# Kernel optimization log

Measured on AMD Instinct MI355X. Metric: run time of the kernel, lower is better.

## Reference

```python
import jax, jax.numpy as jnp
import numpy as np

B, M, C, S, SD, K, H = 32, 448, 384, 512, 128, 8, 8
DH = C // H
EPS = 1e-5
NEG_SLOPE = 0.2


def setup_inputs() -> dict:
    key = jax.random.key(0)
    ks = iter(jax.random.split(key, 32))
    nrm = lambda shape, scale=0.05: (jax.random.normal(next(ks), shape, jnp.float32) * scale)
    inp = {
        'q': jax.random.normal(next(ks), (B, M, C), jnp.float32),
        'coarse': jax.random.normal(next(ks), (B, M, 3), jnp.float32),
        'skeleton': jax.random.normal(next(ks), (B, S, 3), jnp.float32),
        # GraphConv 1: 3 -> 64 (root weight, rel/neighbor weight, bias)
        'gc1_wroot': nrm((3, 64), 0.3), 'gc1_wrel': nrm((3, 64), 0.3), 'gc1_b': jnp.zeros((64,), jnp.float32),
        # GraphConv 2: 64 -> SD
        'gc2_wroot': nrm((64, SD), 0.1), 'gc2_wrel': nrm((64, SD), 0.1), 'gc2_b': jnp.zeros((SD,), jnp.float32),
        # skeleton_projection: SD -> C
        'proj_w': nrm((SD, C), 0.08), 'proj_b': jnp.zeros((C,), jnp.float32),
        # MultiheadAttention (torch layout: in_proj (3C, C), out_proj (C, C))
        'attn_in_w': nrm((3 * C, C), 0.05), 'attn_in_b': jnp.zeros((3 * C,), jnp.float32),
        'attn_out_w': nrm((C, C), 0.05), 'attn_out_b': jnp.zeros((C,), jnp.float32),
        # increase_dim: Conv1d(C,1024,1) + BN(1024) + LeakyReLU + Conv1d(1024,1024,1)
        'inc1_w': nrm((1024, C), 0.05), 'inc1_b': jnp.zeros((1024,), jnp.float32),
        'bn_g': jnp.ones((1024,), jnp.float32), 'bn_b': jnp.zeros((1024,), jnp.float32),
        'bn_m': jnp.zeros((1024,), jnp.float32), 'bn_v': jnp.ones((1024,), jnp.float32),
        'inc2_w': nrm((1024, 1024), 0.03), 'inc2_b': jnp.zeros((1024,), jnp.float32),
        # reduce_map: Linear(C + 1024 + 3, C)
        'red_w': nrm((1024 + C + 3, C), 0.03), 'red_b': jnp.zeros((C,), jnp.float32),
    }
    return inp


def _knn_idx(pts):
    # pts: [B,S,3]; per-batch kNN (self excluded), matching knn_graph(k=K, batch=...)
    d2 = jnp.sum((pts[:, :, None, :] - pts[:, None, :, :]) ** 2, axis=-1)  # [B,S,S]
    d2 = d2 + jnp.eye(S, dtype=pts.dtype)[None] * 1e10                       # mask self
    _, idx = jax.lax.top_k(-d2, K)                                           # [B,S,K]
    return idx


def _graph_conv(x, idx, wroot, wrel, b):
    # GraphConv (PyG, aggr='add'): out_i = x_i Wroot + (sum_{j in N(i)} x_j) Wrel + b
    nb = jax.vmap(lambda f, i: f[i])(x, idx)   # [B,S,K,F]
    agg = nb.sum(axis=2)                       # [B,S,F]
    return x @ wroot + agg @ wrel + b


def reference(q, coarse, skeleton, gc1_wroot, gc1_wrel, gc1_b, gc2_wroot, gc2_wrel, gc2_b,
              proj_w, proj_b, attn_in_w, attn_in_b, attn_out_w, attn_out_b,
              inc1_w, inc1_b, bn_g, bn_b, bn_m, bn_v, inc2_w, inc2_b, red_w, red_b):
    # --- skeleton branch: knn graph + 2-layer GraphConv + max-pool + projection ---
    idx = _knn_idx(skeleton)
    h = _graph_conv(skeleton, idx, gc1_wroot, gc1_wrel, gc1_b)
    h = jax.nn.relu(h)
    h = _graph_conv(h, idx, gc2_wroot, gc2_wrel, gc2_b)        # [B,S,SD]
    proxy = jnp.max(h, axis=1)                                  # [B,SD]
    proxy = proxy @ proj_w + proj_b                             # [B,C]
    kv = jnp.broadcast_to(proxy[:, None, :], (B, M, C))         # expanded proxies

    # --- cross attention (torch nn.MultiheadAttention math) ---
    wq, wk, wv = attn_in_w[:C], attn_in_w[C:2 * C], attn_in_w[2 * C:]
    bq, bk, bv = attn_in_b[:C], attn_in_b[C:2 * C], attn_in_b[2 * C:]
    qh = (q @ wq.T + bq).reshape(B, M, H, DH)
    kh = (kv @ wk.T + bk).reshape(B, M, H, DH)
    vh = (kv @ wv.T + bv).reshape(B, M, H, DH)
    scores = jnp.einsum('bmhd,bnhd->bhmn', qh, kh) / jnp.sqrt(jnp.float32(DH))
    attn = jax.nn.softmax(scores, axis=-1)
    ctx = jnp.einsum('bhmn,bnhd->bmhd', attn, vh).reshape(B, M, C)
    q = ctx @ attn_out_w.T + attn_out_b                         # fused features [B,M,C]

    # --- increase_dim (1x1 conv == matmul) + BN(eval) + LeakyReLU + 1x1 conv ---
    g = jnp.einsum('bmc,oc->bmo', q, inc1_w) + inc1_b           # [B,M,1024]
    g = bn_g * (g - bn_m) * jax.lax.rsqrt(bn_v + EPS) + bn_b
    g = jnp.where(g >= 0, g, NEG_SLOPE * g)
    g = jnp.einsum('bmc,oc->bmo', g, inc2_w) + inc2_b
    global_feature = jnp.max(g, axis=1)                         # [B,1024]

    # --- concat + reduce_map ---
    rebuild = jnp.concatenate([jnp.broadcast_to(global_feature[:, None, :], (B, M, 1024)), q, coarse], axis=-1)
    out = rebuild @ red_w + red_b                               # [B,M,C]
    return out
```

## Files before the change

kernel.cpp:

```cpp
#include <hip/hip_runtime.h>

#define NB 32
#define MM 448
#define CC 384
#define SS 512
#define KNN 8

#define WS_IDX   0u
#define WS_H1    524288u
#define WS_PMAX  (WS_H1 + 4194304u)
#define WS_Q     (WS_PMAX + 262144u)
#define WS_Y     (WS_Q + 49152u)
#define WS_G2    (WS_Y + 131072u)
#define WS_BASEP (WS_G2 + 131072u)
#define WS_PP    WS_H1
#define WS_KV    WS_IDX
#define WS_VV    (WS_IDX + 49152u)

__device__ __forceinline__ float wave_sum(float v) {
#pragma unroll
  for (int m = 1; m < 64; m <<= 1) v += __shfl_xor(v, m, 64);
  return v;
}

__global__ __launch_bounds__(256) void k_knn_gc1(
    const float* __restrict__ skel,
    const float* __restrict__ w1root, const float* __restrict__ w1rel,
    const float* __restrict__ b1,
    int* __restrict__ idx_ws, float* __restrict__ h1_ws)
{
  int b   = blockIdx.x >> 7;
  int grp = blockIdx.x & 127;
  __shared__ __align__(16) float4 sk[SS];
  const float* sb = skel + b * SS * 3;
  for (int t = threadIdx.x; t < SS; t += 256)
    sk[t] = make_float4(sb[t*3+0], sb[t*3+1], sb[t*3+2], 0.f);
  __syncthreads();

  int wave = threadIdx.x >> 6, lane = threadIdx.x & 63;
  int i = grp * 4 + wave;
  float4 pi = sk[i];

  float bd[KNN];
#pragma unroll
  for (int t = 0; t < KNN; t++) {
    int j = lane + (t << 6);
    float4 p = sk[j];
    float d2;
    {
#pragma clang fp contract(off)
      float dx = pi.x - p.x, dy = pi.y - p.y, dz = pi.z - p.z;
      d2 = (dx*dx + dy*dy) + dz*dz;
    }
    bd[t] = (j == i) ? 3e38f : d2;
  }

  int win[KNN];
  int* idx_base = idx_ws + (size_t)(b*SS + i) * KNN;
#pragma unroll
  for (int t = 0; t < KNN; t++) {
    float bestd = bd[0]; int bests = 0;
#pragma unroll
    for (int s = 1; s < KNN; s++)
      if (bd[s] < bestd) { bestd = bd[s]; bests = s; }
    int bestj = lane + (bests << 6);
#pragma unroll
    for (int m = 1; m < 64; m <<= 1) {
      float od = __shfl_xor(bestd, m, 64);
      int   oj = __shfl_xor(bestj, m, 64);
      if (od < bestd || (od == bestd && oj < bestj)) { bestd = od; bestj = oj; }
    }
    win[t] = bestj;
    if (lane == t) idx_base[t] = bestj;
    if ((bestj & 63) == lane) {
      int sl = bestj >> 6;
#pragma unroll
      for (int s = 0; s < KNN; s++) if (s == sl) bd[s] = 3e38f;
    }
  }

  float a0 = 0.f, a1 = 0.f, a2 = 0.f;
#pragma unroll
  for (int t = 0; t < KNN; t++) {
    float4 n = sk[win[t]];
    a0 += n.x; a1 += n.y; a2 += n.z;
  }

  int c = lane;
  float h = b1[c] + pi.x*w1root[c] + pi.y*w1root[64+c] + pi.z*w1root[128+c]
                  + a0*w1rel[c]   + a1*w1rel[64+c]   + a2*w1rel[128+c];
  h = fmaxf(h, 0.f);
  h1_ws[(size_t)(b*SS + i) * 64 + lane] = h;
}

__global__ __launch_bounds__(256) void k_gc2_max(
    const float* __restrict__ h1_ws, const int* __restrict__ idx_ws,
    const float* __restrict__ w2root, const float* __restrict__ w2rel,
    const float* __restrict__ b2, float* __restrict__ pmax)
{
  int b = blockIdx.x >> 4, chunk = blockIdx.x & 15;
  int r0 = chunk * 32;
  __shared__ __align__(16) float X[32*129];
  __shared__ __align__(16) float Wt[32*128];
  __shared__ float mred[8*128];
  __shared__ int nbs[32*KNN];

  const float* h1b = h1_ws + (size_t)b * SS * 64;
  nbs[threadIdx.x] = idx_ws[(b*SS + r0)*KNN + threadIdx.x];
#pragma unroll
  for (int p = 0; p < 8; p++) {
    int idx = threadIdx.x + 256*p;
    int r = idx >> 6, k = idx & 63;
    X[r*129 + k] = h1b[(r0 + r)*64 + k];
  }
  __syncthreads();
#pragma unroll
  for (int p = 0; p < 8; p++) {
    int idx = threadIdx.x + 256*p;
    int r = idx >> 6, k = idx & 63;
    const int* nb = nbs + r*KNN;
    float s = 0.f;
#pragma unroll
    for (int j = 0; j < KNN; j++) s += h1b[nb[j]*64 + k];
    X[r*129 + 64 + k] = s;
  }

  int rg = threadIdx.x >> 5, cg = threadIdx.x & 31;
  float acc[4][4];
#pragma unroll
  for (int r = 0; r < 4; r++)
#pragma unroll
    for (int u = 0; u < 4; u++) acc[r][u] = 0.f;

  const float* wsrc[4] = { w2root, w2root + 32*128, w2rel, w2rel + 32*128 };
#pragma unroll 1
  for (int ch = 0; ch < 4; ch++) {
    __syncthreads();
    const float* ws = wsrc[ch];
#pragma unroll
    for (int p = 0; p < 16; p++) {
      int idx = threadIdx.x + 256*p;
      Wt[idx] = ws[idx];
    }
    __syncthreads();
    int kb = ch * 32;
    const float* xr0 = X + (rg*4+0)*129 + kb;
    const float* xr1 = X + (rg*4+1)*129 + kb;
    const float* xr2 = X + (rg*4+2)*129 + kb;
    const float* xr3 = X + (rg*4+3)*129 + kb;
#pragma unroll 4
    for (int k = 0; k < 32; k++) {
      float4 w4 = *(const float4*)(Wt + k*128 + cg*4);
      float x0 = xr0[k], x1 = xr1[k], x2 = xr2[k], x3 = xr3[k];
      acc[0][0] += x0*w4.x; acc[0][1] += x0*w4.y; acc[0][2] += x0*w4.z; acc[0][3] += x0*w4.w;
      acc[1][0] += x1*w4.x; acc[1][1] += x1*w4.y; acc[1][2] += x1*w4.z; acc[1][3] += x1*w4.w;
      acc[2][0] += x2*w4.x; acc[2][1] += x2*w4.y; acc[2][2] += x2*w4.z; acc[2][3] += x2*w4.w;
      acc[3][0] += x3*w4.x; acc[3][1] += x3*w4.y; acc[3][2] += x3*w4.z; acc[3][3] += x3*w4.w;
    }
  }
#pragma unroll
  for (int u = 0; u < 4; u++)
    mred[rg*128 + cg*4 + u] =
      fmaxf(fmaxf(acc[0][u], acc[1][u]), fmaxf(acc[2][u], acc[3][u]));
  __syncthreads();
  if (threadIdx.x < 128) {
    int col = threadIdx.x;
    float mx = mred[col];
#pragma unroll
    for (int g = 1; g < 8; g++) mx = fmaxf(mx, mred[g*128 + col]);
    pmax[(size_t)(b*16 + chunk)*128 + col] = mx + b2[col];
  }
}

__global__ __launch_bounds__(384) void k_proxy_kv(
    const float* __restrict__ pmax,
    const float* __restrict__ proj_w, const float* __restrict__ proj_b,
    float* __restrict__ kv_ws)
{
  int b = blockIdx.x, t = threadIdx.x;
  __shared__ float proxy[128];
  if (t < 128) {
    float m = -3e38f;
    for (int ch = 0; ch < 16; ch++) m = fmaxf(m, pmax[(size_t)(b*16 + ch)*128 + t]);
    proxy[t] = m;
  }
  __syncthreads();
  float acc = proj_b[t];
  for (int s = 0; s < 128; s++) acc += proxy[s] * proj_w[s*CC + t];
  kv_ws[b*CC + t] = acc;
}

__global__ __launch_bounds__(256) void k_mv384(
    const float* __restrict__ xin, const float* __restrict__ w, int row0,
    const float* __restrict__ bias, int bias0, float* __restrict__ out)
{
  int b = blockIdx.x, og = blockIdx.y;
  int wv = threadIdx.x >> 6, lane = threadIdx.x & 63;
  __shared__ float xs[CC];
  for (int t = threadIdx.x; t < CC; t += 256) xs[t] = xin[b*CC + t];
  __syncthreads();
  float x0 = xs[lane*6+0], x1 = xs[lane*6+1], x2 = xs[lane*6+2];
  float x3 = xs[lane*6+3], x4 = xs[lane*6+4], x5 = xs[lane*6+5];
#pragma unroll
  for (int u = 0; u < 8; u++) {
    int o = og*32 + wv*8 + u;
    const float* wr = w + (size_t)(row0 + o) * CC + lane*6;
    float2 wa = *(const float2*)wr;
    float2 wb = *(const float2*)(wr + 2);
    float2 wc = *(const float2*)(wr + 4);
    float p = wa.x*x0 + wa.y*x1 + wb.x*x2 + wb.y*x3 + wc.x*x4 + wc.y*x5;
    p = wave_sum(p);
    if (lane == 0) out[b*CC + o] = bias[bias0 + o] + p;
  }
}

__global__ __launch_bounds__(256) void k_inc1_bn(
    const float* __restrict__ q_ws, const float* __restrict__ inc1_w,
    const float* __restrict__ inc1_b,
    const float* __restrict__ bng, const float* __restrict__ bnb,
    const float* __restrict__ bnm, const float* __restrict__ bnv,
    float* __restrict__ y_ws)
{
  int b = blockIdx.x >> 4, og = blockIdx.x & 15;
  int t = threadIdx.x;
  int o = og*64 + (t >> 2), qq = t & 3;
  __shared__ __align__(16) float xs[CC];
  for (int i = t; i < CC; i += 256) xs[i] = q_ws[b*CC + i];
  __syncthreads();
  const float* wr = inc1_w + (size_t)o * CC + qq*96;
  const float* xr = xs + qq*96;
  float acc = 0.f;
#pragma unroll
  for (int kk = 0; kk < 96; kk += 4) {
    float4 w4 = *(const float4*)(wr + kk);
    float4 x4 = *(const float4*)(xr + kk);
    acc += w4.x*x4.x + w4.y*x4.y + w4.z*x4.z + w4.w*x4.w;
  }
  acc += __shfl_xor(acc, 1, 64);
  acc += __shfl_xor(acc, 2, 64);
  if (qq == 0) {
    float a = acc + inc1_b[o];
    float z = bng[o] * (a - bnm[o]) * rsqrtf(bnv[o] + 1e-5f) + bnb[o];
    y_ws[b*1024 + o] = (z >= 0.f) ? z : 0.2f * z;
  }
}

__global__ __launch_bounds__(256) void k_inc2(
    const float* __restrict__ y_ws, const float* __restrict__ inc2_w,
    const float* __restrict__ inc2_b, float* __restrict__ g2_ws)
{
  int b = blockIdx.x >> 4, og = blockIdx.x & 15;
  int t = threadIdx.x;
  int o = og*64 + (t >> 2), qq = t & 3;
  __shared__ __align__(16) float xs[1024];
  for (int i = t; i < 1024; i += 256) xs[i] = y_ws[b*1024 + i];
  __syncthreads();
  const float* wr = inc2_w + (size_t)o * 1024 + qq*256;
  const float* xr = xs + qq*256;
  float acc = 0.f;
#pragma unroll 8
  for (int kk = 0; kk < 256; kk += 4) {
    float4 w4 = *(const float4*)(wr + kk);
    float4 x4 = *(const float4*)(xr + kk);
    acc += w4.x*x4.x + w4.y*x4.y + w4.z*x4.z + w4.w*x4.w;
  }
  acc += __shfl_xor(acc, 1, 64);
  acc += __shfl_xor(acc, 2, 64);
  if (qq == 0) g2_ws[b*1024 + o] = acc + inc2_b[o];
}

__global__ __launch_bounds__(256) void k_basep(
    const float* __restrict__ g2_ws, const float* __restrict__ q_ws,
    const float* __restrict__ red_w, float* __restrict__ pp)
{
  int cg = blockIdx.x;
  int o0 = blockIdx.y * 64;
  int c0 = cg * 32;
  __shared__ __align__(16) float xs[32*33];
  __shared__ __align__(16) float wt[32*64];
#pragma unroll
  for (int p = 0; p < 8; p++) {
    int idx = threadIdx.x + 256*p;
    int c = idx >> 6, o = idx & 63;
    wt[idx] = red_w[(size_t)(c0 + c)*CC + o0 + o];
  }
  {
    int b = threadIdx.x >> 3, cp = threadIdx.x & 7;
    const float* src = (cg < 32) ? (g2_ws + b*1024 + c0)
                                 : (q_ws  + b*CC   + (c0 - 1024));
    float4 v = *(const float4*)(src + cp*4);
    xs[(cp*4+0)*33 + b] = v.x;
    xs[(cp*4+1)*33 + b] = v.y;
    xs[(cp*4+2)*33 + b] = v.z;
    xs[(cp*4+3)*33 + b] = v.w;
  }
  __syncthreads();
  int b = threadIdx.x >> 3, og = threadIdx.x & 7;
  float acc[8];
#pragma unroll
  for (int u = 0; u < 8; u++) acc[u] = 0.f;
#pragma unroll 8
  for (int c = 0; c < 32; c++) {
    float xv = xs[c*33 + b];
    float4 w0 = *(const float4*)(wt + c*64 + og*8);
    float4 w1 = *(const float4*)(wt + c*64 + og*8 + 4);
    acc[0] += xv*w0.x; acc[1] += xv*w0.y; acc[2] += xv*w0.z; acc[3] += xv*w0.w;
    acc[4] += xv*w1.x; acc[5] += xv*w1.y; acc[6] += xv*w1.z; acc[7] += xv*w1.w;
  }
  float* dst = pp + (size_t)(cg*32 + b)*CC + o0 + og*8;
  *(float4*)dst       = make_float4(acc[0], acc[1], acc[2], acc[3]);
  *(float4*)(dst + 4) = make_float4(acc[4], acc[5], acc[6], acc[7]);
}

__global__ __launch_bounds__(256) void k_base_red(
    const float* __restrict__ pp, float* __restrict__ basep)
{
  int idx = blockIdx.x * 256 + threadIdx.x;
  float s = 0.f;
#pragma unroll 4
  for (int cg = 0; cg < 44; cg++) s += pp[cg*12288 + idx];
  basep[idx] = s;
}

__global__ __launch_bounds__(256) void k_out(
    const float* __restrict__ basep, const float* __restrict__ red_b,
    const float* __restrict__ red_w, const float* __restrict__ coarse,
    float* __restrict__ out)
{
  int gid = blockIdx.x * 256 + threadIdx.x;
  int c4 = gid % 96;
  int row = gid / 96;
  int b = row / 448;
  int c = c4 * 4;
  float4 p0 = *(const float4*)(basep + b*CC + c);
  float4 rb = *(const float4*)(red_b + c);
  const float* cr = coarse + (size_t)row * 3;
  float cx = cr[0], cy = cr[1], cz = cr[2];
  float4 w0 = *(const float4*)(red_w + (size_t)1408*CC + c);
  float4 w1 = *(const float4*)(red_w + (size_t)1409*CC + c);
  float4 w2 = *(const float4*)(red_w + (size_t)1410*CC + c);
  float4 o4;
  o4.x = p0.x + rb.x + cx*w0.x + cy*w1.x + cz*w2.x;
  o4.y = p0.y + rb.y + cx*w0.y + cy*w1.y + cz*w2.y;
  o4.z = p0.z + rb.z + cx*w0.z + cy*w1.z + cz*w2.z;
  o4.w = p0.w + rb.w + cx*w0.w + cy*w1.w + cz*w2.w;
  *(float4*)(out + (size_t)row*CC + c) = o4;
}

extern "C" void kernel_launch(void* const* d_in, const int* in_sizes, int n_in,
                              void* d_out, int out_size, void* d_ws, size_t ws_size,
                              hipStream_t stream)
{
  (void)in_sizes; (void)n_in; (void)out_size; (void)ws_size;
  const float* coarse = (const float*)d_in[1];
  const float* skel   = (const float*)d_in[2];
  const float* g1wr   = (const float*)d_in[3];
  const float* g1wl   = (const float*)d_in[4];
  const float* g1b    = (const float*)d_in[5];
  const float* g2wr   = (const float*)d_in[6];
  const float* g2wl   = (const float*)d_in[7];
  const float* g2b    = (const float*)d_in[8];
  const float* projw  = (const float*)d_in[9];
  const float* projb  = (const float*)d_in[10];
  const float* aiw    = (const float*)d_in[11];
  const float* aib    = (const float*)d_in[12];
  const float* aow    = (const float*)d_in[13];
  const float* aob    = (const float*)d_in[14];
  const float* i1w    = (const float*)d_in[15];
  const float* i1b    = (const float*)d_in[16];
  const float* bng    = (const float*)d_in[17];
  const float* bnb    = (const float*)d_in[18];
  const float* bnm    = (const float*)d_in[19];
  const float* bnv    = (const float*)d_in[20];
  const float* i2w    = (const float*)d_in[21];
  const float* i2b    = (const float*)d_in[22];
  const float* redw   = (const float*)d_in[23];
  const float* redb   = (const float*)d_in[24];
  float* out = (float*)d_out;

  char* ws = (char*)d_ws;
  int*   idx_ws = (int*)(ws + WS_IDX);
  float* h1_ws  = (float*)(ws + WS_H1);
  float* pmax   = (float*)(ws + WS_PMAX);
  float* q_ws   = (float*)(ws + WS_Q);
  float* y_ws   = (float*)(ws + WS_Y);
  float* g2_ws  = (float*)(ws + WS_G2);
  float* basep  = (float*)(ws + WS_BASEP);
  float* pp     = (float*)(ws + WS_PP);
  float* kv_ws  = (float*)(ws + WS_KV);
  float* vv_ws  = (float*)(ws + WS_VV);

  k_knn_gc1<<<4096, 256, 0, stream>>>(skel, g1wr, g1wl, g1b, idx_ws, h1_ws);
  k_gc2_max<<<512, 256, 0, stream>>>(h1_ws, idx_ws, g2wr, g2wl, g2b, pmax);
  k_proxy_kv<<<32, 384, 0, stream>>>(pmax, projw, projb, kv_ws);
  k_mv384<<<dim3(32, 12), 256, 0, stream>>>(kv_ws, aiw, 2*CC, aib, 2*CC, vv_ws);
  k_mv384<<<dim3(32, 12), 256, 0, stream>>>(vv_ws, aow, 0,    aob, 0,    q_ws);
  k_inc1_bn<<<512, 256, 0, stream>>>(q_ws, i1w, i1b, bng, bnb, bnm, bnv, y_ws);
  k_inc2<<<512, 256, 0, stream>>>(y_ws, i2w, i2b, g2_ws);
  k_basep<<<dim3(44, 6), 256, 0, stream>>>(g2_ws, q_ws, redw, pp);
  k_base_red<<<48, 256, 0, stream>>>(pp, basep);
  k_out<<<5376, 256, 0, stream>>>(basep, redb, redw, coarse, out);
}
```

Measured before the change: 236.0 us.

## Fuse post-kNN stages into one persistent kernel with software grid barriers

Nine launches after the kNN/GraphConv1 kernel are merged into one 512-block kernel whose stages are separated by atomic-counter grid barriers. The aim is to remove per-launch overhead and tail gaps between small dependent kernels. The reduce_map partial-sum scheme (44 chunks written out, then a separate reduction) is replaced by 48 blocks that each loop over the full concatenated input, writing the reduction directly. The software barrier assumes all 512 blocks are co-resident, which launch_bounds(256,2) is meant to make likely on this GPU. Barrier spinning and poorly utilised stages (48 active blocks) are the costs taken on.

```diff
diff --git a/kernel.cpp b/kernel.cpp
--- a/kernel.cpp
+++ b/kernel.cpp
@@ -5,30 +5,49 @@
 #define CC 384
 #define SS 512
 #define KNN 8
-
-#define WS_IDX   0u
-#define WS_H1    524288u
-#define WS_PMAX  (WS_H1 + 4194304u)
-#define WS_Q     (WS_PMAX + 262144u)
-#define WS_Y     (WS_Q + 49152u)
-#define WS_G2    (WS_Y + 131072u)
-#define WS_BASEP (WS_G2 + 131072u)
-#define WS_PP    WS_H1
-#define WS_KV    WS_IDX
-#define WS_VV    (WS_IDX + 49152u)
+#define NBLK 512u
+
+#define WS_IDX    0u
+#define WS_H1     524288u
+#define WS_PMAX   4718592u
+#define WS_VV     4980736u
+#define WS_Y      5029888u
+#define WS_XCAT   5160960u
+#define WS_BASEP  5341184u
+#define WS_BAR    5390336u
 
 __device__ __forceinline__ float wave_sum(float v) {
 #pragma unroll
   for (int m = 1; m < 64; m <<= 1) v += __shfl_xor(v, m, 64);
   return v;
+}
+
+__device__ __forceinline__ void gbar(unsigned* c) {
+  __threadfence();
+  __syncthreads();
+  if (threadIdx.x == 0) {
+    __hip_atomic_fetch_add(c, 1u, __ATOMIC_RELEASE, __HIP_MEMORY_SCOPE_AGENT);
+    long spins = 0;
+    unsigned v;
+    do {
+      v = __hip_atomic_load(c, __ATOMIC_ACQUIRE, __HIP_MEMORY_SCOPE_AGENT);
+      if (v >= NBLK) break;
+      __builtin_amdgcn_s_sleep(1);
+    } while (++spins < (1L << 27));
+  }
+  __syncthreads();
+  __threadfence();
 }
 
 __global__ __launch_bounds__(256) void k_knn_gc1(
     const float* __restrict__ skel,
     const float* __restrict__ w1root, const float* __restrict__ w1rel,
     const float* __restrict__ b1,
-    int* __restrict__ idx_ws, float* __restrict__ h1_ws)
+    int* __restrict__ idx_ws, float* __restrict__ h1_ws,
+    unsigned* __restrict__ bar)
 {
+  if (blockIdx.x == 0 && threadIdx.x < 6) bar[threadIdx.x * 16] = 0u;
+
   int b   = blockIdx.x >> 7;
   int grp = blockIdx.x & 127;
   __shared__ __align__(16) float4 sk[SS];
@@ -93,258 +112,264 @@
   h1_ws[(size_t)(b*SS + i) * 64 + lane] = h;
 }
 
-__global__ __launch_bounds__(256) void k_gc2_max(
-    const float* __restrict__ h1_ws, const int* __restrict__ idx_ws,
-    const float* __restrict__ w2root, const float* __restrict__ w2rel,
-    const float* __restrict__ b2, float* __restrict__ pmax)
+struct CoopArgs {
+  const float* h1; const int* idx;
+  const float *g2wr, *g2wl, *g2b;
+  const float *projw, *projb;
+  const float *aiw, *aib, *aow, *aob;
+  const float *i1w, *i1b, *bng, *bnb, *bnm, *bnv;
+  const float *i2w, *i2b;
+  const float *redw, *redb;
+  const float* coarse;
+  float *pmax, *vv, *y, *xcat, *basep, *out;
+  unsigned* bar;
+};
+
+__global__ __launch_bounds__(256, 2) void k_fused(CoopArgs a)
 {
-  int b = blockIdx.x >> 4, chunk = blockIdx.x & 15;
-  int r0 = chunk * 32;
-  __shared__ __align__(16) float X[32*129];
-  __shared__ __align__(16) float Wt[32*128];
-  __shared__ float mred[8*128];
-  __shared__ int nbs[32*KNN];
-
-  const float* h1b = h1_ws + (size_t)b * SS * 64;
-  nbs[threadIdx.x] = idx_ws[(b*SS + r0)*KNN + threadIdx.x];
-#pragma unroll
-  for (int p = 0; p < 8; p++) {
-    int idx = threadIdx.x + 256*p;
-    int r = idx >> 6, k = idx & 63;
-    X[r*129 + k] = h1b[(r0 + r)*64 + k];
-  }
-  __syncthreads();
-#pragma unroll
-  for (int p = 0; p < 8; p++) {
-    int idx = threadIdx.x + 256*p;
-    int r = idx >> 6, k = idx & 63;
-    const int* nb = nbs + r*KNN;
-    float s = 0.f;
-#pragma unroll
-    for (int j = 0; j < KNN; j++) s += h1b[nb[j]*64 + k];
-    X[r*129 + 64 + k] = s;
-  }
-
-  int rg = threadIdx.x >> 5, cg = threadIdx.x & 31;
-  float acc[4][4];
-#pragma unroll
-  for (int r = 0; r < 4; r++)
-#pragma unroll
-    for (int u = 0; u < 4; u++) acc[r][u] = 0.f;
-
-  const float* wsrc[4] = { w2root, w2root + 32*128, w2rel, w2rel + 32*128 };
+  __shared__ __align__(16) float smem[9600];
+  const int t   = threadIdx.x;
+  const int blk = blockIdx.x;
+
+  {
+    int b = blk >> 4, chunk = blk & 15;
+    int r0 = chunk * 32;
+    float* X    = smem;
+    float* Wt   = smem + 4128;
+    float* mred = smem + 8224;
+    int*   nbs  = (int*)(smem + 9248);
+
+    const float* h1b = a.h1 + (size_t)b * SS * 64;
+    nbs[t] = a.idx[(b*SS + r0)*KNN + t];
+#pragma unroll
+    for (int p = 0; p < 8; p++) {
+      int idx = t + 256*p;
+      int r = idx >> 6, k = idx & 63;
+      X[r*129 + k] = h1b[(r0 + r)*64 + k];
+    }
+    __syncthreads();
+#pragma unroll
+    for (int p = 0; p < 8; p++) {
+      int idx = t + 256*p;
+      int r = idx >> 6, k = idx & 63;
+      const int* nb = nbs + r*KNN;
+      float s = 0.f;
+#pragma unroll
+      for (int j = 0; j < KNN; j++) s += h1b[nb[j]*64 + k];
+      X[r*129 + 64 + k] = s;
+    }
+
+    int rg = t >> 5, cgi = t & 31;
+    float acc[4][4];
+#pragma unroll
+    for (int r = 0; r < 4; r++)
+#pragma unroll
+      for (int u = 0; u < 4; u++) acc[r][u] = 0.f;
+
+    const float* wsrc[4] = { a.g2wr, a.g2wr + 32*128, a.g2wl, a.g2wl + 32*128 };
 #pragma unroll 1
-  for (int ch = 0; ch < 4; ch++) {
-    __syncthreads();
-    const float* ws = wsrc[ch];
-#pragma unroll
-    for (int p = 0; p < 16; p++) {
-      int idx = threadIdx.x + 256*p;
-      Wt[idx] = ws[idx];
-    }
-    __syncthreads();
-    int kb = ch * 32;
-    const float* xr0 = X + (rg*4+0)*129 + kb;
-    const float* xr1 = X + (rg*4+1)*129 + kb;
-    const float* xr2 = X + (rg*4+2)*129 + kb;
-    const float* xr3 = X + (rg*4+3)*129 + kb;
+    for (int ch = 0; ch < 4; ch++) {
+      __syncthreads();
+      const float* ws = wsrc[ch];
+#pragma unroll
+      for (int p = 0; p < 16; p++) {
+        int idx = t + 256*p;
+        Wt[idx] = ws[idx];
+      }
+      __syncthreads();
+      int kb = ch * 32;
+      const float* xr0 = X + (rg*4+0)*129 + kb;
+      const float* xr1 = X + (rg*4+1)*129 + kb;
+      const float* xr2 = X + (rg*4+2)*129 + kb;
+      const float* xr3 = X + (rg*4+3)*129 + kb;
 #pragma unroll 4
-    for (int k = 0; k < 32; k++) {
-      float4 w4 = *(const float4*)(Wt + k*128 + cg*4);
-      float x0 = xr0[k], x1 = xr1[k], x2 = xr2[k], x3 = xr3[k];
-      acc[0][0] += x0*w4.x; acc[0][1] += x0*w4.y; acc[0][2] += x0*w4.z; acc[0][3] += x0*w4.w;
-      acc[1][0] += x1*w4.x; acc[1][1] += x1*w4.y; acc[1][2] += x1*w4.z; acc[1][3] += x1*w4.w;
-      acc[2][0] += x2*w4.x; acc[2][1] += x2*w4.y; acc[2][2] += x2*w4.z; acc[2][3] += x2*w4.w;
-      acc[3][0] += x3*w4.x; acc[3][1] += x3*w4.y; acc[3][2] += x3*w4.z; acc[3][3] += x3*w4.w;
-    }
-  }
-#pragma unroll
-  for (int u = 0; u < 4; u++)
-    mred[rg*128 + cg*4 + u] =
-      fmaxf(fmaxf(acc[0][u], acc[1][u]), fmaxf(acc[2][u], acc[3][u]));
-  __syncthreads();
-  if (threadIdx.x < 128) {
-    int col = threadIdx.x;
-    float mx = mred[col];
-#pragma unroll
-    for (int g = 1; g < 8; g++) mx = fmaxf(mx, mred[g*128 + col]);
-    pmax[(size_t)(b*16 + chunk)*128 + col] = mx + b2[col];
-  }
-}
-
-__global__ __launch_bounds__(384) void k_proxy_kv(
-    const float* __restrict__ pmax,
-    const float* __restrict__ proj_w, const float* __restrict__ proj_b,
-    float* __restrict__ kv_ws)
-{
-  int b = blockIdx.x, t = threadIdx.x;
-  __shared__ float proxy[128];
-  if (t < 128) {
-    float m = -3e38f;
-    for (int ch = 0; ch < 16; ch++) m = fmaxf(m, pmax[(size_t)(b*16 + ch)*128 + t]);
-    proxy[t] = m;
-  }
-  __syncthreads();
-  float acc = proj_b[t];
-  for (int s = 0; s < 128; s++) acc += proxy[s] * proj_w[s*CC + t];
-  kv_ws[b*CC + t] = acc;
-}
-
-__global__ __launch_bounds__(256) void k_mv384(
-    const float* __restrict__ xin, const float* __restrict__ w, int row0,
-    const float* __restrict__ bias, int bias0, float* __restrict__ out)
-{
-  int b = blockIdx.x, og = blockIdx.y;
-  int wv = threadIdx.x >> 6, lane = threadIdx.x & 63;
-  __shared__ float xs[CC];
-  for (int t = threadIdx.x; t < CC; t += 256) xs[t] = xin[b*CC + t];
-  __syncthreads();
-  float x0 = xs[lane*6+0], x1 = xs[lane*6+1], x2 = xs[lane*6+2];
-  float x3 = xs[lane*6+3], x4 = xs[lane*6+4], x5 = xs[lane*6+5];
-#pragma unroll
-  for (int u = 0; u < 8; u++) {
-    int o = og*32 + wv*8 + u;
-    const float* wr = w + (size_t)(row0 + o) * CC + lane*6;
-    float2 wa = *(const float2*)wr;
-    float2 wb = *(const float2*)(wr + 2);
-    float2 wc = *(const float2*)(wr + 4);
-    float p = wa.x*x0 + wa.y*x1 + wb.x*x2 + wb.y*x3 + wc.x*x4 + wc.y*x5;
-    p = wave_sum(p);
-    if (lane == 0) out[b*CC + o] = bias[bias0 + o] + p;
-  }
-}
-
-__global__ __launch_bounds__(256) void k_inc1_bn(
-    const float* __restrict__ q_ws, const float* __restrict__ inc1_w,
-    const float* __restrict__ inc1_b,
-    const float* __restrict__ bng, const float* __restrict__ bnb,
-    const float* __restrict__ bnm, const float* __restrict__ bnv,
-    float* __restrict__ y_ws)
-{
-  int b = blockIdx.x >> 4, og = blockIdx.x & 15;
-  int t = threadIdx.x;
-  int o = og*64 + (t >> 2), qq = t & 3;
-  __shared__ __align__(16) float xs[CC];
-  for (int i = t; i < CC; i += 256) xs[i] = q_ws[b*CC + i];
-  __syncthreads();
-  const float* wr = inc1_w + (size_t)o * CC + qq*96;
-  const float* xr = xs + qq*96;
-  float acc = 0.f;
-#pragma unroll
-  for (int kk = 0; kk < 96; kk += 4) {
-    float4 w4 = *(const float4*)(wr + kk);
-    float4 x4 = *(const float4*)(xr + kk);
-    acc += w4.x*x4.x + w4.y*x4.y + w4.z*x4.z + w4.w*x4.w;
-  }
-  acc += __shfl_xor(acc, 1, 64);
-  acc += __shfl_xor(acc, 2, 64);
-  if (qq == 0) {
-    float a = acc + inc1_b[o];
-    float z = bng[o] * (a - bnm[o]) * rsqrtf(bnv[o] + 1e-5f) + bnb[o];
-    y_ws[b*1024 + o] = (z >= 0.f) ? z : 0.2f * z;
-  }
-}
-
-__global__ __launch_bounds__(256) void k_inc2(
-    const float* __restrict__ y_ws, const float* __restrict__ inc2_w,
-    const float* __restrict__ inc2_b, float* __restrict__ g2_ws)
-{
-  int b = blockIdx.x >> 4, og = blockIdx.x & 15;
-  int t = threadIdx.x;
-  int o = og*64 + (t >> 2), qq = t & 3;
-  __shared__ __align__(16) float xs[1024];
-  for (int i = t; i < 1024; i += 256) xs[i] = y_ws[b*1024 + i];
-  __syncthreads();
-  const float* wr = inc2_w + (size_t)o * 1024 + qq*256;
-  const float* xr = xs + qq*256;
-  float acc = 0.f;
+      for (int k = 0; k < 32; k++) {
+        float4 w4 = *(const float4*)(Wt + k*128 + cgi*4);
+        float x0 = xr0[k], x1 = xr1[k], x2 = xr2[k], x3 = xr3[k];
+        acc[0][0] += x0*w4.x; acc[0][1] += x0*w4.y; acc[0][2] += x0*w4.z; acc[0][3] += x0*w4.w;
+        acc[1][0] += x1*w4.x; acc[1][1] += x1*w4.y; acc[1][2] += x1*w4.z; acc[1][3] += x1*w4.w;
+        acc[2][0] += x2*w4.x; acc[2][1] += x2*w4.y; acc[2][2] += x2*w4.z; acc[2][3] += x2*w4.w;
+        acc[3][0] += x3*w4.x; acc[3][1] += x3*w4.y; acc[3][2] += x3*w4.z; acc[3][3] += x3*w4.w;
+      }
+    }
+#pragma unroll
+    for (int u = 0; u < 4; u++)
+      mred[rg*128 + cgi*4 + u] =
+        fmaxf(fmaxf(acc[0][u], acc[1][u]), fmaxf(acc[2][u], acc[3][u]));
+    __syncthreads();
+    if (t < 128) {
+      float mx = mred[t];
+#pragma unroll
+      for (int g = 1; g < 8; g++) mx = fmaxf(mx, mred[g*128 + t]);
+      a.pmax[(size_t)(b*16 + chunk)*128 + t] = mx + a.g2b[t];
+    }
+  }
+  gbar(a.bar + 0*16);
+
+  if (blk < 384) {
+    int b = blk & 31, og = blk >> 5;
+    if (t < 128) {
+      float m = -3e38f;
+      for (int ch = 0; ch < 16; ch++)
+        m = fmaxf(m, a.pmax[(size_t)(b*16 + ch)*128 + t]);
+      smem[t] = m;
+    }
+    __syncthreads();
+    for (int o = t; o < CC; o += 256) {
+      float acc = a.projb[o];
+      for (int s = 0; s < 128; s++) acc += smem[s] * a.projw[s*CC + o];
+      smem[128 + o] = acc;
+    }
+    __syncthreads();
+    const float* xs = smem + 128;
+    int wv = t >> 6, lane = t & 63;
+    float x0 = xs[lane*6+0], x1 = xs[lane*6+1], x2 = xs[lane*6+2];
+    float x3 = xs[lane*6+3], x4 = xs[lane*6+4], x5 = xs[lane*6+5];
+#pragma unroll
+    for (int u = 0; u < 8; u++) {
+      int o = og*32 + wv*8 + u;
+      const float* wr = a.aiw + (size_t)(2*CC + o) * CC + lane*6;
+      float2 wa = *(const float2*)wr;
+      float2 wb = *(const float2*)(wr + 2);
+      float2 wc = *(const float2*)(wr + 4);
+      float p = wa.x*x0 + wa.y*x1 + wb.x*x2 + wb.y*x3 + wc.x*x4 + wc.y*x5;
+      p = wave_sum(p);
+      if (lane == 0) a.vv[b*CC + o] = a.aib[2*CC + o] + p;
+    }
+  }
+  gbar(a.bar + 1*16);
+
+  if (blk < 384) {
+    int b = blk & 31, og = blk >> 5;
+    for (int i = t; i < CC; i += 256) smem[i] = a.vv[b*CC + i];
+    __syncthreads();
+    int wv = t >> 6, lane = t & 63;
+    float x0 = smem[lane*6+0], x1 = smem[lane*6+1], x2 = smem[lane*6+2];
+    float x3 = smem[lane*6+3], x4 = smem[lane*6+4], x5 = smem[lane*6+5];
+#pragma unroll
+    for (int u = 0; u < 8; u++) {
+      int o = og*32 + wv*8 + u;
+      const float* wr = a.aow + (size_t)o * CC + lane*6;
+      float2 wa = *(const float2*)wr;
+      float2 wb = *(const float2*)(wr + 2);
+      float2 wc = *(const float2*)(wr + 4);
+      float p = wa.x*x0 + wa.y*x1 + wb.x*x2 + wb.y*x3 + wc.x*x4 + wc.y*x5;
+      p = wave_sum(p);
+      if (lane == 0) a.xcat[b*1408 + 1024 + o] = a.aob[o] + p;
+    }
+  }
+  gbar(a.bar + 2*16);
+
+  {
+    int b = blk >> 4, og = blk & 15;
+    int o = og*64 + (t >> 2), qq = t & 3;
+    for (int i = t; i < CC; i += 256) smem[i] = a.xcat[b*1408 + 1024 + i];
+    __syncthreads();
+    const float* wr = a.i1w + (size_t)o * CC + qq*96;
+    const float* xr = smem + qq*96;
+    float acc = 0.f;
+#pragma unroll
+    for (int kk = 0; kk < 96; kk += 4) {
+      float4 w4 = *(const float4*)(wr + kk);
+      float4 x4 = *(const float4*)(xr + kk);
+      acc += w4.x*x4.x + w4.y*x4.y + w4.z*x4.z + w4.w*x4.w;
+    }
+    acc += __shfl_xor(acc, 1, 64);
+    acc += __shfl_xor(acc, 2, 64);
+    if (qq == 0) {
+      float v = acc + a.i1b[o];
+      float z = a.bng[o] * (v - a.bnm[o]) * rsqrtf(a.bnv[o] + 1e-5f) + a.bnb[o];
+      a.y[b*1024 + o] = (z >= 0.f) ? z : 0.2f * z;
+    }
+  }
+  gbar(a.bar + 3*16);
+
+  {
+    int b = blk >> 4, og = blk & 15;
+    int o = og*64 + (t >> 2), qq = t & 3;
+    for (int i = t; i < 1024; i += 256) smem[i] = a.y[b*1024 + i];
+    __syncthreads();
+    const float* wr = a.i2w + (size_t)o * 1024 + qq*256;
+    const float* xr = smem + qq*256;
+    float acc = 0.f;
 #pragma unroll 8
-  for (int kk = 0; kk < 256; kk += 4) {
-    float4 w4 = *(const float4*)(wr + kk);
-    float4 x4 = *(const float4*)(xr + kk);
-    acc += w4.x*x4.x + w4.y*x4.y + w4.z*x4.z + w4.w*x4.w;
-  }
-  acc += __shfl_xor(acc, 1, 64);
-  acc += __shfl_xor(acc, 2, 64);
-  if (qq == 0) g2_ws[b*1024 + o] = acc + inc2_b[o];
-}
-
-__global__ __launch_bounds__(256) void k_basep(
-    const float* __restrict__ g2_ws, const float* __restrict__ q_ws,
-    const float* __restrict__ red_w, float* __restrict__ pp)
-{
-  int cg = blockIdx.x;
-  int o0 = blockIdx.y * 64;
-  int c0 = cg * 32;
-  __shared__ __align__(16) float xs[32*33];
-  __shared__ __align__(16) float wt[32*64];
-#pragma unroll
-  for (int p = 0; p < 8; p++) {
-    int idx = threadIdx.x + 256*p;
-    int c = idx >> 6, o = idx & 63;
-    wt[idx] = red_w[(size_t)(c0 + c)*CC + o0 + o];
-  }
+    for (int kk = 0; kk < 256; kk += 4) {
+      float4 w4 = *(const float4*)(wr + kk);
+      float4 x4 = *(const float4*)(xr + kk);
+      acc += w4.x*x4.x + w4.y*x4.y + w4.z*x4.z + w4.w*x4.w;
+    }
+    acc += __shfl_xor(acc, 1, 64);
+    acc += __shfl_xor(acc, 2, 64);
+    if (qq == 0) a.xcat[b*1408 + o] = acc + a.i2b[o];
+  }
+  gbar(a.bar + 4*16);
+
+  if (blk < 48) {
+    int o0 = blk * 8;
+    float* xs = smem;
+    float* wt = smem + 4128;
+    int o4 = t & 1, bb = (t >> 1) & 31, kq = t >> 6;
+    float acc0 = 0.f, acc1 = 0.f, acc2 = 0.f, acc3 = 0.f;
+#pragma unroll 1
+    for (int c0 = 0; c0 < 1408; c0 += 128) {
+      __syncthreads();
+#pragma unroll
+      for (int p = 0; p < 16; p++) {
+        int idx = t + 256*p;
+        xs[(idx >> 7)*129 + (idx & 127)] = a.xcat[(idx >> 7)*1408 + c0 + (idx & 127)];
+      }
+#pragma unroll
+      for (int p = 0; p < 4; p++) {
+        int idx = t + 256*p;
+        wt[idx] = a.redw[(size_t)(c0 + (idx >> 3)) * CC + o0 + (idx & 7)];
+      }
+      __syncthreads();
+      const float* xrow = xs + bb*129 + kq*32;
+      const float* wrow = wt + kq*32*8 + o4*4;
+#pragma unroll 8
+      for (int i = 0; i < 32; i++) {
+        float  x  = xrow[i];
+        float4 w4 = *(const float4*)(wrow + i*8);
+        acc0 += x*w4.x; acc1 += x*w4.y; acc2 += x*w4.z; acc3 += x*w4.w;
+      }
+    }
+    __syncthreads();
+    float* red = smem;
+    red[t*4+0] = acc0; red[t*4+1] = acc1; red[t*4+2] = acc2; red[t*4+3] = acc3;
+    __syncthreads();
+    {
+      int bb2 = t >> 3, oj = t & 7;
+      float s = 0.f;
+#pragma unroll
+      for (int k2 = 0; k2 < 4; k2++)
+        s += red[(k2*64 + bb2*2 + (oj >> 2))*4 + (oj & 3)];
+      a.basep[bb2*CC + o0 + oj] = s;
+    }
+  }
+  gbar(a.bar + 5*16);
+
   {
-    int b = threadIdx.x >> 3, cp = threadIdx.x & 7;
-    const float* src = (cg < 32) ? (g2_ws + b*1024 + c0)
-                                 : (q_ws  + b*CC   + (c0 - 1024));
-    float4 v = *(const float4*)(src + cp*4);
-    xs[(cp*4+0)*33 + b] = v.x;
-    xs[(cp*4+1)*33 + b] = v.y;
-    xs[(cp*4+2)*33 + b] = v.z;
-    xs[(cp*4+3)*33 + b] = v.w;
-  }
-  __syncthreads();
-  int b = threadIdx.x >> 3, og = threadIdx.x & 7;
-  float acc[8];
-#pragma unroll
-  for (int u = 0; u < 8; u++) acc[u] = 0.f;
-#pragma unroll 8
-  for (int c = 0; c < 32; c++) {
-    float xv = xs[c*33 + b];
-    float4 w0 = *(const float4*)(wt + c*64 + og*8);
-    float4 w1 = *(const float4*)(wt + c*64 + og*8 + 4);
-    acc[0] += xv*w0.x; acc[1] += xv*w0.y; acc[2] += xv*w0.z; acc[3] += xv*w0.w;
-    acc[4] += xv*w1.x; acc[5] += xv*w1.y; acc[6] += xv*w1.z; acc[7] += xv*w1.w;
-  }
-  float* dst = pp + (size_t)(cg*32 + b)*CC + o0 + og*8;
-  *(float4*)dst       = make_float4(acc[0], acc[1], acc[2], acc[3]);
-  *(float4*)(dst + 4) = make_float4(acc[4], acc[5], acc[6], acc[7]);
-}
-
-__global__ __launch_bounds__(256) void k_base_red(
-    const float* __restrict__ pp, float* __restrict__ basep)
-{
-  int idx = blockIdx.x * 256 + threadIdx.x;
-  float s = 0.f;
-#pragma unroll 4
-  for (int cg = 0; cg < 44; cg++) s += pp[cg*12288 + idx];
-  basep[idx] = s;
-}
-
-__global__ __launch_bounds__(256) void k_out(
-    const float* __restrict__ basep, const float* __restrict__ red_b,
-    const float* __restrict__ red_w, const float* __restrict__ coarse,
-    float* __restrict__ out)
-{
-  int gid = blockIdx.x * 256 + threadIdx.x;
-  int c4 = gid % 96;
-  int row = gid / 96;
-  int b = row / 448;
-  int c = c4 * 4;
-  float4 p0 = *(const float4*)(basep + b*CC + c);
-  float4 rb = *(const float4*)(red_b + c);
-  const float* cr = coarse + (size_t)row * 3;
-  float cx = cr[0], cy = cr[1], cz = cr[2];
-  float4 w0 = *(const float4*)(red_w + (size_t)1408*CC + c);
-  float4 w1 = *(const float4*)(red_w + (size_t)1409*CC + c);
-  float4 w2 = *(const float4*)(red_w + (size_t)1410*CC + c);
-  float4 o4;
-  o4.x = p0.x + rb.x + cx*w0.x + cy*w1.x + cz*w2.x;
-  o4.y = p0.y + rb.y + cx*w0.y + cy*w1.y + cz*w2.y;
-  o4.z = p0.z + rb.z + cx*w0.z + cy*w1.z + cz*w2.z;
-  o4.w = p0.w + rb.w + cx*w0.w + cy*w1.w + cz*w2.w;
-  *(float4*)(out + (size_t)row*CC + c) = o4;
+    const int total = NB*MM*96;
+    for (int gid = blk*256 + t; gid < total; gid += (int)NBLK*256) {
+      int c4 = gid % 96;
+      int row = gid / 96;
+      int b = row / 448;
+      int c = c4 * 4;
+      float4 p0 = *(const float4*)(a.basep + b*CC + c);
+      float4 rb = *(const float4*)(a.redb + c);
+      const float* cr = a.coarse + (size_t)row * 3;
+      float cx = cr[0], cy = cr[1], cz = cr[2];
+      float4 w0 = *(const float4*)(a.redw + (size_t)1408*CC + c);
+      float4 w1 = *(const float4*)(a.redw + (size_t)1409*CC + c);
+      float4 w2 = *(const float4*)(a.redw + (size_t)1410*CC + c);
+      float4 o4v;
+      o4v.x = p0.x + rb.x + cx*w0.x + cy*w1.x + cz*w2.x;
+      o4v.y = p0.y + rb.y + cx*w0.y + cy*w1.y + cz*w2.y;
+      o4v.z = p0.z + rb.z + cx*w0.z + cy*w1.z + cz*w2.z;
+      o4v.w = p0.w + rb.w + cx*w0.w + cy*w1.w + cz*w2.w;
+      *(float4*)(a.out + (size_t)row*CC + c) = o4v;
+    }
+  }
 }
 
 extern "C" void kernel_launch(void* const* d_in, const int* in_sizes, int n_in,
@@ -357,47 +382,43 @@
   const float* g1wr   = (const float*)d_in[3];
   const float* g1wl   = (const float*)d_in[4];
   const float* g1b    = (const float*)d_in[5];
-  const float* g2wr   = (const float*)d_in[6];
-  const float* g2wl   = (const float*)d_in[7];
-  const float* g2b    = (const float*)d_in[8];
-  const float* projw  = (const float*)d_in[9];
-  const float* projb  = (const float*)d_in[10];
-  const float* aiw    = (const float*)d_in[11];
-  const float* aib    = (const float*)d_in[12];
-  const float* aow    = (const float*)d_in[13];
-  const float* aob    = (const float*)d_in[14];
-  const float* i1w    = (const float*)d_in[15];
-  const float* i1b    = (const float*)d_in[16];
-  const float* bng    = (const float*)d_in[17];
-  const float* bnb    = (const float*)d_in[18];
-  const float* bnm    = (const float*)d_in[19];
-  const float* bnv    = (const float*)d_in[20];
-  const float* i2w    = (const float*)d_in[21];
-  const float* i2b    = (const float*)d_in[22];
-  const float* redw   = (const float*)d_in[23];
-  const float* redb   = (const float*)d_in[24];
-  float* out = (float*)d_out;
 
   char* ws = (char*)d_ws;
-  int*   idx_ws = (int*)(ws + WS_IDX);
-  float* h1_ws  = (float*)(ws + WS_H1);
-  float* pmax   = (float*)(ws + WS_PMAX);
-  float* q_ws   = (float*)(ws + WS_Q);
-  float* y_ws   = (float*)(ws + WS_Y);
-  float* g2_ws  = (float*)(ws + WS_G2);
-  float* basep  = (float*)(ws + WS_BASEP);
-  float* pp     = (float*)(ws + WS_PP);
-  float* kv_ws  = (float*)(ws + WS_KV);
-  float* vv_ws  = (float*)(ws + WS_VV);
-
-  k_knn_gc1<<<4096, 256, 0, stream>>>(skel, g1wr, g1wl, g1b, idx_ws, h1_ws);
-  k_gc2_max<<<512, 256, 0, stream>>>(h1_ws, idx_ws, g2wr, g2wl, g2b, pmax);
-  k_proxy_kv<<<32, 384, 0, stream>>>(pmax, projw, projb, kv_ws);
-  k_mv384<<<dim3(32, 12), 256, 0, stream>>>(kv_ws, aiw, 2*CC, aib, 2*CC, vv_ws);
-  k_mv384<<<dim3(32, 12), 256, 0, stream>>>(vv_ws, aow, 0,    aob, 0,    q_ws);
-  k_inc1_bn<<<512, 256, 0, stream>>>(q_ws, i1w, i1b, bng, bnb, bnm, bnv, y_ws);
-  k_inc2<<<512, 256, 0, stream>>>(y_ws, i2w, i2b, g2_ws);
-  k_basep<<<dim3(44, 6), 256, 0, stream>>>(g2_ws, q_ws, redw, pp);
-  k_base_red<<<48, 256, 0, stream>>>(pp, basep);
-  k_out<<<5376, 256, 0, stream>>>(basep, redb, redw, coarse, out);
+  int*      idx_ws = (int*)(ws + WS_IDX);
+  float*    h1_ws  = (float*)(ws + WS_H1);
+  unsigned* bar    = (unsigned*)(ws + WS_BAR);
+
+  CoopArgs a;
+  a.h1    = h1_ws;
+  a.idx   = idx_ws;
+  a.g2wr  = (const float*)d_in[6];
+  a.g2wl  = (const float*)d_in[7];
+  a.g2b   = (const float*)d_in[8];
+  a.projw = (const float*)d_in[9];
+  a.projb = (const float*)d_in[10];
+  a.aiw   = (const float*)d_in[11];
+  a.aib   = (const float*)d_in[12];
+  a.aow   = (const float*)d_in[13];
+  a.aob   = (const float*)d_in[14];
+  a.i1w   = (const float*)d_in[15];
+  a.i1b   = (const float*)d_in[16];
+  a.bng   = (const float*)d_in[17];
+  a.bnb   = (const float*)d_in[18];
+  a.bnm   = (const float*)d_in[19];
+  a.bnv   = (const float*)d_in[20];
+  a.i2w   = (const float*)d_in[21];
+  a.i2b   = (const float*)d_in[22];
+  a.redw  = (const float*)d_in[23];
+  a.redb  = (const float*)d_in[24];
+  a.coarse= coarse;
+  a.pmax  = (float*)(ws + WS_PMAX);
+  a.vv    = (float*)(ws + WS_VV);
+  a.y     = (float*)(ws + WS_Y);
+  a.xcat  = (float*)(ws + WS_XCAT);
+  a.basep = (float*)(ws + WS_BASEP);
+  a.out   = (float*)d_out;
+  a.bar   = bar;
+
+  k_knn_gc1<<<4096, 256, 0, stream>>>(skel, g1wr, g1wl, g1b, idx_ws, h1_ws, bar);
+  k_fused<<<NBLK, 256, 0, stream>>>(a);
 }
```

Result: slower. 933.3 us (+295.4%).

## Fuse proxy projection with V projection and merge basep partial-sum reduction

Applied to the files above, without the earlier changes.

Combines the skeleton proxy projection and the V in-projection into one kernel, where each block recomputes the 384-wide kv vector in shared memory before its matvec slice. Replaces the two-kernel split-K reduce_map base computation, which wrote and re-read a 44x32x384 partial buffer, with a single kernel that loops over all 1408 input channels and reduces inside the block. This removes two launches and the partial-sum traffic. In exchange the proxy projection is computed redundantly (12x), and the new basep kernel runs only 48 blocks, each with a long serial K loop.

```diff
diff --git a/kernel.cpp b/kernel.cpp
--- a/kernel.cpp
+++ b/kernel.cpp
@@ -6,16 +6,14 @@
 #define SS 512
 #define KNN 8
 
-#define WS_IDX   0u
-#define WS_H1    524288u
-#define WS_PMAX  (WS_H1 + 4194304u)
-#define WS_Q     (WS_PMAX + 262144u)
-#define WS_Y     (WS_Q + 49152u)
-#define WS_G2    (WS_Y + 131072u)
-#define WS_BASEP (WS_G2 + 131072u)
-#define WS_PP    WS_H1
-#define WS_KV    WS_IDX
-#define WS_VV    (WS_IDX + 49152u)
+#define WS_IDX    0u
+#define WS_H1     524288u
+#define WS_PMAX   4718592u
+#define WS_VV     4980736u
+#define WS_Q      5029888u
+#define WS_Y      5079040u
+#define WS_G2     5210112u
+#define WS_BASEP  5341184u
 
 __device__ __forceinline__ float wave_sum(float v) {
 #pragma unroll
@@ -172,22 +170,45 @@
   }
 }
 
-__global__ __launch_bounds__(384) void k_proxy_kv(
+__global__ __launch_bounds__(256) void k_chain1(
     const float* __restrict__ pmax,
     const float* __restrict__ proj_w, const float* __restrict__ proj_b,
-    float* __restrict__ kv_ws)
-{
-  int b = blockIdx.x, t = threadIdx.x;
+    const float* __restrict__ aiw, const float* __restrict__ aib,
+    float* __restrict__ vv_ws)
+{
+  int b = blockIdx.x & 31, og = blockIdx.x >> 5;
   __shared__ float proxy[128];
+  __shared__ float kv[CC];
+  int t = threadIdx.x;
   if (t < 128) {
     float m = -3e38f;
-    for (int ch = 0; ch < 16; ch++) m = fmaxf(m, pmax[(size_t)(b*16 + ch)*128 + t]);
+    const float* pm = pmax + (size_t)b*2048 + t;
+#pragma unroll
+    for (int ch = 0; ch < 16; ch++) m = fmaxf(m, pm[ch*128]);
     proxy[t] = m;
   }
   __syncthreads();
-  float acc = proj_b[t];
-  for (int s = 0; s < 128; s++) acc += proxy[s] * proj_w[s*CC + t];
-  kv_ws[b*CC + t] = acc;
+  for (int o = t; o < CC; o += 256) {
+    float acc = proj_b[o];
+#pragma unroll 8
+    for (int k = 0; k < 128; k++) acc += proxy[k] * proj_w[k*CC + o];
+    kv[o] = acc;
+  }
+  __syncthreads();
+  int wv = t >> 6, lane = t & 63;
+  float x0 = kv[lane*6+0], x1 = kv[lane*6+1], x2 = kv[lane*6+2];
+  float x3 = kv[lane*6+3], x4 = kv[lane*6+4], x5 = kv[lane*6+5];
+#pragma unroll
+  for (int u = 0; u < 8; u++) {
+    int o = og*32 + wv*8 + u;
+    const float* wr = aiw + (size_t)(2*CC + o) * CC + lane*6;
+    float2 wa = *(const float2*)wr;
+    float2 wb = *(const float2*)(wr + 2);
+    float2 wc = *(const float2*)(wr + 4);
+    float p = wa.x*x0 + wa.y*x1 + wb.x*x2 + wb.y*x3 + wc.x*x4 + wc.y*x5;
+    p = wave_sum(p);
+    if (lane == 0) vv_ws[b*CC + o] = aib[2*CC + o] + p;
+  }
 }
 
 __global__ __launch_bounds__(256) void k_mv384(
@@ -269,57 +290,54 @@
   if (qq == 0) g2_ws[b*1024 + o] = acc + inc2_b[o];
 }
 
-__global__ __launch_bounds__(256) void k_basep(
+__global__ __launch_bounds__(256) void k_basep_full(
     const float* __restrict__ g2_ws, const float* __restrict__ q_ws,
-    const float* __restrict__ red_w, float* __restrict__ pp)
-{
-  int cg = blockIdx.x;
-  int o0 = blockIdx.y * 64;
-  int c0 = cg * 32;
-  __shared__ __align__(16) float xs[32*33];
-  __shared__ __align__(16) float wt[32*64];
-#pragma unroll
-  for (int p = 0; p < 8; p++) {
-    int idx = threadIdx.x + 256*p;
-    int c = idx >> 6, o = idx & 63;
-    wt[idx] = red_w[(size_t)(c0 + c)*CC + o0 + o];
-  }
+    const float* __restrict__ red_w, float* __restrict__ basep)
+{
+  int o0 = blockIdx.x * 8;
+  __shared__ __align__(16) float xs[32*129];
+  __shared__ __align__(16) float wt[128*8];
+  int t = threadIdx.x;
+  int o4 = t & 1, bb = (t >> 1) & 31, kq = t >> 6;
+  float acc0 = 0.f, acc1 = 0.f, acc2 = 0.f, acc3 = 0.f;
+#pragma unroll 1
+  for (int c0 = 0; c0 < 1408; c0 += 128) {
+    __syncthreads();
+    const float* src = (c0 < 1024) ? (g2_ws + c0) : (q_ws + (c0 - 1024));
+    int stride = (c0 < 1024) ? 1024 : CC;
+#pragma unroll
+    for (int p = 0; p < 16; p++) {
+      int idx = t + 256*p;
+      int b = idx >> 7, k = idx & 127;
+      xs[b*129 + k] = src[(size_t)b*stride + k];
+    }
+#pragma unroll
+    for (int p = 0; p < 4; p++) {
+      int idx = t + 256*p;
+      wt[idx] = red_w[(size_t)(c0 + (idx >> 3)) * CC + o0 + (idx & 7)];
+    }
+    __syncthreads();
+    const float* xrow = xs + bb*129 + kq*32;
+    const float* wrow = wt + kq*32*8 + o4*4;
+#pragma unroll 8
+    for (int i = 0; i < 32; i++) {
+      float  x  = xrow[i];
+      float4 w4 = *(const float4*)(wrow + i*8);
+      acc0 += x*w4.x; acc1 += x*w4.y; acc2 += x*w4.z; acc3 += x*w4.w;
+    }
+  }
+  __syncthreads();
+  float* red = xs;
+  red[t*4+0] = acc0; red[t*4+1] = acc1; red[t*4+2] = acc2; red[t*4+3] = acc3;
+  __syncthreads();
   {
-    int b = threadIdx.x >> 3, cp = threadIdx.x & 7;
-    const float* src = (cg < 32) ? (g2_ws + b*1024 + c0)
-                                 : (q_ws  + b*CC   + (c0 - 1024));
-    float4 v = *(const float4*)(src + cp*4);
-    xs[(cp*4+0)*33 + b] = v.x;
-    xs[(cp*4+1)*33 + b] = v.y;
-    xs[(cp*4+2)*33 + b] = v.z;
-    xs[(cp*4+3)*33 + b] = v.w;
-  }
-  __syncthreads();
-  int b = threadIdx.x >> 3, og = threadIdx.x & 7;
-  float acc[8];
-#pragma unroll
-  for (int u = 0; u < 8; u++) acc[u] = 0.f;
-#pragma unroll 8
-  for (int c = 0; c < 32; c++) {
-    float xv = xs[c*33 + b];
-    float4 w0 = *(const float4*)(wt + c*64 + og*8);
-    float4 w1 = *(const float4*)(wt + c*64 + og*8 + 4);
-    acc[0] += xv*w0.x; acc[1] += xv*w0.y; acc[2] += xv*w0.z; acc[3] += xv*w0.w;
-    acc[4] += xv*w1.x; acc[5] += xv*w1.y; acc[6] += xv*w1.z; acc[7] += xv*w1.w;
-  }
-  float* dst = pp + (size_t)(cg*32 + b)*CC + o0 + og*8;
-  *(float4*)dst       = make_float4(acc[0], acc[1], acc[2], acc[3]);
-  *(float4*)(dst + 4) = make_float4(acc[4], acc[5], acc[6], acc[7]);
-}
-
-__global__ __launch_bounds__(256) void k_base_red(
-    const float* __restrict__ pp, float* __restrict__ basep)
-{
-  int idx = blockIdx.x * 256 + threadIdx.x;
-  float s = 0.f;
-#pragma unroll 4
-  for (int cg = 0; cg < 44; cg++) s += pp[cg*12288 + idx];
-  basep[idx] = s;
+    int bb2 = t >> 3, oj = t & 7;
+    float s = 0.f;
+#pragma unroll
+    for (int k2 = 0; k2 < 4; k2++)
+      s += red[(k2*64 + bb2*2 + (oj >> 2))*4 + (oj & 3)];
+    basep[bb2*CC + o0 + oj] = s;
+  }
 }
 
 __global__ __launch_bounds__(256) void k_out(
@@ -382,22 +400,18 @@
   int*   idx_ws = (int*)(ws + WS_IDX);
   float* h1_ws  = (float*)(ws + WS_H1);
   float* pmax   = (float*)(ws + WS_PMAX);
+  float* vv_ws  = (float*)(ws + WS_VV);
   float* q_ws   = (float*)(ws + WS_Q);
   float* y_ws   = (float*)(ws + WS_Y);
   float* g2_ws  = (float*)(ws + WS_G2);
   float* basep  = (float*)(ws + WS_BASEP);
-  float* pp     = (float*)(ws + WS_PP);
-  float* kv_ws  = (float*)(ws + WS_KV);
-  float* vv_ws  = (float*)(ws + WS_VV);
 
   k_knn_gc1<<<4096, 256, 0, stream>>>(skel, g1wr, g1wl, g1b, idx_ws, h1_ws);
   k_gc2_max<<<512, 256, 0, stream>>>(h1_ws, idx_ws, g2wr, g2wl, g2b, pmax);
-  k_proxy_kv<<<32, 384, 0, stream>>>(pmax, projw, projb, kv_ws);
-  k_mv384<<<dim3(32, 12), 256, 0, stream>>>(kv_ws, aiw, 2*CC, aib, 2*CC, vv_ws);
-  k_mv384<<<dim3(32, 12), 256, 0, stream>>>(vv_ws, aow, 0,    aob, 0,    q_ws);
+  k_chain1<<<384, 256, 0, stream>>>(pmax, projw, projb, aiw, aib, vv_ws);
+  k_mv384<<<dim3(32, 12), 256, 0, stream>>>(vv_ws, aow, 0, aob, 0, q_ws);
   k_inc1_bn<<<512, 256, 0, stream>>>(q_ws, i1w, i1b, bng, bnb, bnm, bnv, y_ws);
   k_inc2<<<512, 256, 0, stream>>>(y_ws, i2w, i2b, g2_ws);
-  k_basep<<<dim3(44, 6), 256, 0, stream>>>(g2_ws, q_ws, redw, pp);
-  k_base_red<<<48, 256, 0, stream>>>(pp, basep);
+  k_basep_full<<<48, 256, 0, stream>>>(g2_ws, q_ws, redw, basep);
   k_out<<<5376, 256, 0, stream>>>(basep, redb, redw, coarse, out);
 }
```

Result: slower. 282.4 us (+19.7%).
